# Kernel tuning notes

Hardware: AMD Instinct MI355X
Metric: run time of the kernel (lower is better)

## Reference

```python
import jax, jax.numpy as jnp
import numpy as np

B, STEP, H, N_ENC = 256, 32, 512, 60
PD, LD, NB, NTYPE, NPLAYER = 32, 32, 6, 11, 35


def _parity_masks(S):
    # Static relation-11/12 edge masks from update_adjacency_matrix (step is a Python int).
    m11 = np.zeros((S, S), dtype=bool)
    m12 = np.zeros((S, S), dtype=bool)
    for row in range(S):
        ni = row // 2
        if row % 2 == 0:
            c = (ni + 1) * 2
            if c <= S - 1:
                (m11 if ni % 2 == 0 else m12)[row, c] = True
                (m11 if ni % 2 == 0 else m12)[c, row] = True
        else:
            c = (ni + 1) * 2 + 1
            if c <= S - 1:
                (m12 if ni % 2 == 0 else m11)[row, c] = True
                (m12 if ni % 2 == 0 else m11)[c, row] = True
    return jnp.asarray(m11), jnp.asarray(m12)


def update_adjacency(adj, step, shot_type_predict=False):
    b = adj.shape[0]
    S = step * 2
    new = jnp.zeros((b, 13, S, S), dtype=adj.dtype).at[:, :, :S - 2, :S - 2].set(adj)
    m11, m12 = _parity_masks(S)
    new = new.at[:, 11].set(jnp.where(m11, 1, new[:, 11]))
    new = new.at[:, 12].set(jnp.where(m12, 1, new[:, 12]))
    if shot_type_predict:
        idx = (step - 1) * 2 if step % 2 == 0 else (step - 1) * 2 + 1
        new = new.at[:, :, idx, :].set(0).at[:, :, :, idx].set(0)
    return new


def rgcn(node, adj, layer_params):
    # adj: (B,13,N,N) int; slice off relation 0 -> 12 relations. Dropout is eval-mode identity.
    adj_f = adj[:, 1:].astype(node.dtype)  # (B,12,N,N)
    x = node
    n_layers = len(layer_params)
    for i, (basis, comb, w_self) in enumerate(layer_params):
        act = jax.nn.sigmoid if i == n_layers - 1 else jax.nn.relu
        W = jnp.einsum('rb,bij->rij', comb, basis)            # (12,H,H)
        msg = jnp.einsum('brnm,bmh->brnh', adj_f, x)          # (B,12,N,H)
        x = act(jnp.einsum('brnh,rhk->bnk', msg, W) + x @ w_self.T)
    return x


def setup_inputs() -> dict:
    key = jax.random.key(0)
    ks = jax.random.split(key, 20)
    s = 0.05
    return {
        'player': jax.random.randint(ks[0], (B, 2), 0, NPLAYER, dtype=jnp.int32),
        'step': STEP,
        'encode_node_embedding': jax.random.normal(ks[1], (B, N_ENC, H), jnp.float32),
        'adjacency_matrix': jax.random.randint(ks[2], (B, 13, (STEP - 1) * 2, (STEP - 1) * 2), 0, 2, dtype=jnp.int32),
        'player_A_x': jax.random.uniform(ks[3], (B, 1), jnp.float32),
        'player_A_y': jax.random.uniform(ks[4], (B, 1), jnp.float32),
        'player_B_x': jax.random.uniform(ks[5], (B, 1), jnp.float32),
        'player_B_y': jax.random.uniform(ks[6], (B, 1), jnp.float32),
        'emb_table': jax.random.normal(ks[7], (NPLAYER, PD), jnp.float32) * s,
        'coord_W': jax.random.normal(ks[8], (LD, 2), jnp.float32) * s,
        'coord_b': jnp.zeros((LD,), jnp.float32),
        'in_W': jax.random.normal(ks[9], (H, PD + LD), jnp.float32) * s,
        'in_b': jnp.zeros((H,), jnp.float32),
        'basis0': jax.random.normal(ks[10], (NB, H, H), jnp.float32) * s,
        'comb0': jax.random.normal(ks[11], (12, NB), jnp.float32) * s,
        'self0': jax.random.normal(ks[12], (H, H), jnp.float32) * s,
        'basis1': jax.random.normal(ks[13], (NB, H, H), jnp.float32) * s,
        'comb1': jax.random.normal(ks[14], (12, NB), jnp.float32) * s,
        'self1': jax.random.normal(ks[15], (H, H), jnp.float32) * s,
        'type_W': jax.random.normal(ks[16], (NTYPE, 2 * H), jnp.float32) * s,
        'type_b': jnp.zeros((NTYPE,), jnp.float32),
    }


def reference(player, step, encode_node_embedding, adjacency_matrix,
              player_A_x, player_A_y, player_B_x, player_B_y,
              emb_table, coord_W, coord_b, in_W, in_b,
              basis0, comb0, self0, basis1, comb1, self1, type_W, type_b):
    b = player.shape[0]
    layers = [(basis0, comb0, self0), (basis1, comb1, self1)]

    coord_A = jnp.stack([player_A_x, player_A_y], axis=2)   # (B,1,2)
    coord_B = jnp.stack([player_B_x, player_B_y], axis=2)   # (B,1,2)
    coords = jnp.stack([coord_A, coord_B], axis=2).reshape(b, -1, 2)  # (B,2,2)
    loc = jax.nn.relu(coords @ coord_W.T + coord_b)          # (B,2,LD)
    pemb = emb_table[player]                                 # (B,2,PD)
    initial = jnp.concatenate([loc, pemb], axis=-1) @ in_W.T + in_b  # (B,2,H)

    # first=False branch: current coords == prev coords, so model_input == initial
    mi = jnp.concatenate([encode_node_embedding, initial], axis=1)   # (B,62,H)
    tmp = rgcn(mi, adjacency_matrix, layers)
    passed = jnp.concatenate([encode_node_embedding[:, :-2], tmp[:, -4:]], axis=1)  # (B,62,H)

    tmp_adj = update_adjacency(adjacency_matrix, step, shot_type_predict=True)  # (B,13,64,64)
    mi2 = jnp.concatenate([passed, initial], axis=1)         # (B,64,H)
    drop = (step - 1) * 2 if step % 2 == 0 else (step - 1) * 2 + 1
    keep = np.delete(np.arange(step * 2), drop)
    mi2 = mi2[:, keep]
    tmp_adj = tmp_adj[:, :, keep][:, :, :, keep]
    tmp2 = rgcn(mi2, tmp_adj, layers)                        # (B,63,H)

    pad = jnp.zeros((b, tmp2.shape[1] + 1, tmp2.shape[2]), tmp2.dtype)
    if step % 2 == 0:
        pad = pad.at[:, :-2].set(tmp2[:, :-1]).at[:, -1].set(tmp2[:, -1])
    else:
        pad = pad.at[:, :-1].set(tmp2)
    stp = jnp.concatenate([passed[:, :-2], pad[:, -4:]], axis=1)  # (B,64,H)
    if step % 2 == 0:
        black = stp[:, (step - 1) * 2 + 1]
        white = stp[:, (step - 2) * 2]
    else:
        black = stp[:, (step - 2) * 2 + 1]
        white = stp[:, (step - 1) * 2]
    logits = jnp.concatenate([black, white], axis=-1) @ type_W.T + type_b
    return logits
```

## Files before the change

### kernel.cpp

```cpp
#include <hip/hip_runtime.h>
#include <hip/hip_bf16.h>

typedef unsigned short u16;
typedef unsigned long long u64;
typedef __attribute__((ext_vector_type(4))) short short4v;
typedef __attribute__((ext_vector_type(8))) short short8;
typedef __attribute__((ext_vector_type(4))) float floatx4;

__device__ __forceinline__ u16 f2bf(float f) {
    union { float f; unsigned u; } v; v.f = f;
    unsigned r = v.u + 0x7FFF + ((v.u >> 16) & 1);
    return (u16)(r >> 16);
}

__global__ void k_wcat(const float* __restrict__ basis, const float* __restrict__ selfW,
                       u16* __restrict__ wf) {
    int bi = blockIdx.x, t = threadIdx.x;
    int kr = t >> 7;
    int nb = (t & 127) * 4;
    for (int it = 0; it < 4; ++it) {
        int k = bi * 8 + it * 2 + kr;
        float v0, v1, v2, v3;
        if (k < 3072) {
            int q = k >> 9, h = k & 511;
            const float4 bz = *(const float4*)(basis + ((size_t)(q * 512 + h)) * 512 + nb);
            v0 = bz.x; v1 = bz.y; v2 = bz.z; v3 = bz.w;
        } else {
            int kk = k - 3072;
            v0 = selfW[(size_t)(nb + 0) * 512 + kk];
            v1 = selfW[(size_t)(nb + 1) * 512 + kk];
            v2 = selfW[(size_t)(nb + 2) * 512 + kk];
            v3 = selfW[(size_t)(nb + 3) * 512 + kk];
        }
        float vv[4] = {v0, v1, v2, v3};
        for (int i = 0; i < 4; ++i) {
            int n = nb + i;
            wf[(size_t)(k >> 5) * 16384 + (n >> 4) * 512 + ((k >> 3) & 3) * 128 + (n & 15) * 8 + (k & 7)] = f2bf(vv[i]);
        }
    }
}

__global__ void k_masks(const int* __restrict__ A, u64* __restrict__ m0, u64* __restrict__ m1) {
    int bi = blockIdx.x;
    int b = bi / 12, r = bi % 12;
    const int* Ab = A + (size_t)(b * 13 + (r + 1)) * 62 * 62;
    int lane = threadIdx.x;
    u64 my0 = 0, my1 = 0;
    for (int n = 0; n < 64; ++n) {
        int raw = 0;
        if (n < 62 && lane < 62) raw = (Ab[n * 62 + lane] != 0) ? 1 : 0;
        u64 b0 = __ballot(raw != 0);
        int v1 = 0;
        if (n < 63 && lane < 63) {
            int oi = (n == 62) ? 63 : n;
            int oj = (lane == 62) ? 63 : lane;
            v1 = (oi < 62 && oj < 62) ? raw : 0;
            int lo = (oi < oj) ? oi : oj, hi = (oi < oj) ? oj : oi;
            if (hi == lo + 2) {
                int p = (lo >> 1) & 1;
                int chp = ((lo & 1) == 0) ? (p ? 12 : 11) : (p ? 11 : 12);
                if (r + 1 == chp) v1 = 1;
            }
        }
        u64 b1 = __ballot(v1 != 0);
        if (lane == n) { my0 = b0; my1 = b1; }
    }
    m0[(size_t)bi * 64 + lane] = my0;
    m1[(size_t)bi * 64 + lane] = my1;
}

#define AQ_SETSTRIDE (256UL * 6 * 4096)
__global__ void k_aqexp(const u64* __restrict__ msk, const float* __restrict__ comb0,
                        const float* __restrict__ comb1, u16* __restrict__ aq) {
    int b = blockIdx.x >> 3, sp = blockIdx.x & 7;
    int t = threadIdx.x;
    __shared__ u64 sm[12 * 64];
    __shared__ float cmb[2][12][6];
    if (t < 72) { cmb[0][t / 6][t % 6] = comb0[t]; cmb[1][t / 6][t % 6] = comb1[t]; }
    for (int i = t; i < 768; i += 256) sm[i] = msk[(size_t)b * 768 + i];
    __syncthreads();
    #pragma unroll
    for (int ii2 = 0; ii2 < 2; ++ii2) {
        int pos = (sp * 2 + ii2) * 256 + t;
        int f = pos >> 9, lane = (pos >> 3) & 63, j = pos & 7;
        int row = ((f >> 1) << 4) + (lane & 15);
        int mb  = ((f & 1) << 5) + ((lane >> 4) << 3) + j;
        float bits[12];
        #pragma unroll
        for (int r = 0; r < 12; ++r) bits[r] = (float)((sm[r * 64 + row] >> mb) & 1ull);
        #pragma unroll
        for (int s = 0; s < 2; ++s)
            #pragma unroll
            for (int q = 0; q < 6; ++q) {
                float v = 0.f;
                #pragma unroll
                for (int r = 0; r < 12; ++r) v += bits[r] * cmb[s][r][q];
                aq[(size_t)s * AQ_SETSTRIDE + ((size_t)b * 6 + q) * 4096 + pos] = f2bf(v);
            }
    }
}

__global__ void k_prep(const int* __restrict__ player,
                       const float* __restrict__ pAx, const float* __restrict__ pAy,
                       const float* __restrict__ pBx, const float* __restrict__ pBy,
                       const float* __restrict__ emb, const float* __restrict__ cW,
                       const float* __restrict__ cb, const float* __restrict__ inW,
                       const float* __restrict__ inb,
                       u16* __restrict__ mi1, u16* __restrict__ mi2) {
    int b = blockIdx.x, t = threadIdx.x;
    __shared__ float feat[2][64];
    if (t < 64) {
        int j = t >> 5, d = t & 31;
        float X = j ? pBx[b] : pAx[b];
        float Y = j ? pBy[b] : pAy[b];
        feat[j][d] = fmaxf(cW[d * 2] * X + cW[d * 2 + 1] * Y + cb[d], 0.f);
        feat[j][32 + d] = emb[player[b * 2 + j] * 32 + d];
    }
    __syncthreads();
    for (int h = t; h < 512; h += 256) {
        float a0 = inb[h], a1 = inb[h];
        const float* wrow = inW + h * 64;
        #pragma unroll
        for (int d = 0; d < 64; ++d) {
            float wv = wrow[d];
            a0 += wv * feat[0][d];
            a1 += wv * feat[1][d];
        }
        u16 v0 = f2bf(a0), v1 = f2bf(a1);
        size_t base = (size_t)b * 64 * 512;
        mi1[base + 60 * 512 + h] = v0;
        mi1[base + 61 * 512 + h] = v1;
        mi1[base + 62 * 512 + h] = 0;
        mi1[base + 63 * 512 + h] = 0;
        mi2[base + 62 * 512 + h] = v1;
        mi2[base + 63 * 512 + h] = 0;
    }
}

__global__ void k_cast(const float* __restrict__ enc, u16* __restrict__ mi1, u16* __restrict__ mi2) {
    long long e = ((long long)blockIdx.x * 256 + threadIdx.x) * 8;
    if (e >= 256LL * 60 * 512) return;
    int b = (int)(e / (60 * 512));
    int rm = (int)(e % (60 * 512));
    int n = rm / 512, h = rm % 512;
    for (int i = 0; i < 8; ++i) {
        u16 v = f2bf(enc[e + i]);
        mi1[((size_t)b * 64 + n) * 512 + h + i] = v;
        if (n < 58) mi2[((size_t)b * 64 + n) * 512 + h + i] = v;
    }
}

__global__ __launch_bounds__(512, 2)
void k_layer(const u16* __restrict__ x, const u16* __restrict__ aq,
             const u16* __restrict__ wc, u16* __restrict__ out) {
    int b = blockIdx.x >> 1, nh = blockIdx.x & 1;
    int t = threadIdx.x, lane = t & 63, w = t >> 6;
    int l15 = lane & 15, lq = lane >> 4;
    const int TS = 520;
    __shared__ __align__(16) u16 T[64 * 520];

    const u16* xb_base = x + (size_t)b * 64 * 512;
    short8 xb[8];
    #pragma unroll
    for (int nt = 0; nt < 4; ++nt)
        #pragma unroll
        for (int kh = 0; kh < 2; ++kh) {
            int h = (w * 4 + nt) * 16 + l15;
            int j0 = kh * 32 + lq * 8;
            short8 v;
            #pragma unroll
            for (int jj = 0; jj < 8; ++jj)
                v[jj] = (short)xb_base[(size_t)(j0 + jj) * 512 + h];
            xb[nt * 2 + kh] = v;
        }

    floatx4 acc[8];
    #pragma unroll
    for (int i = 0; i < 8; ++i) acc[i] = (floatx4)(0.f);

    const u16* aqb   = aq + (size_t)b * 6 * 4096 + (size_t)lane * 8;
    const u16* wbase = wc + (size_t)lane * 8;
    int cf0 = nh * 16 + w * 2;

    for (int q = 0; q < 6; ++q) {
        __syncthreads();
        for (int i = 0; i < 4; ++i) {
            short8 a0 = *(const short8*)(aqb + (size_t)q * 4096 + (i * 2 + 0) * 512);
            short8 a1 = *(const short8*)(aqb + (size_t)q * 4096 + (i * 2 + 1) * 512);
            #pragma unroll
            for (int nt = 0; nt < 4; ++nt) {
                floatx4 tz = (floatx4)(0.f);
                tz = __builtin_amdgcn_mfma_f32_16x16x32_bf16(a0, xb[nt * 2 + 0], tz, 0, 0, 0);
                tz = __builtin_amdgcn_mfma_f32_16x16x32_bf16(a1, xb[nt * 2 + 1], tz, 0, 0, 0);
                int hcol = (w * 4 + nt) * 16 + l15;
                int mrow = i * 16 + lq * 4;
                #pragma unroll
                for (int reg = 0; reg < 4; ++reg)
                    T[(mrow + reg) * TS + hcol] = f2bf(tz[reg]);
            }
        }
        __syncthreads();
        for (int ks = 0; ks < 16; ++ks) {
            short8 af[4], bf[2];
            #pragma unroll
            for (int i = 0; i < 4; ++i)
                af[i] = *(const short8*)&T[(i * 16 + l15) * TS + ks * 32 + lq * 8];
            #pragma unroll
            for (int nt = 0; nt < 2; ++nt)
                bf[nt] = *(const short8*)(wbase + (size_t)(q * 16 + ks) * 16384 + (size_t)(cf0 + nt) * 512);
            #pragma unroll
            for (int i = 0; i < 4; ++i)
                #pragma unroll
                for (int nt = 0; nt < 2; ++nt)
                    acc[i * 2 + nt] = __builtin_amdgcn_mfma_f32_16x16x32_bf16(af[i], bf[nt], acc[i * 2 + nt], 0, 0, 0);
        }
    }
    for (int ks = 0; ks < 16; ++ks) {
        short8 af[4], bf[2];
        #pragma unroll
        for (int i = 0; i < 4; ++i)
            af[i] = *(const short8*)(xb_base + (size_t)(i * 16 + l15) * 512 + ks * 32 + lq * 8);
        #pragma unroll
        for (int nt = 0; nt < 2; ++nt)
            bf[nt] = *(const short8*)(wbase + (size_t)(96 + ks) * 16384 + (size_t)(cf0 + nt) * 512);
        #pragma unroll
        for (int i = 0; i < 4; ++i)
            #pragma unroll
            for (int nt = 0; nt < 2; ++nt)
                acc[i * 2 + nt] = __builtin_amdgcn_mfma_f32_16x16x32_bf16(af[i], bf[nt], acc[i * 2 + nt], 0, 0, 0);
    }
    #pragma unroll
    for (int i = 0; i < 4; ++i)
        #pragma unroll
        for (int nt = 0; nt < 2; ++nt) {
            int n = nh * 256 + w * 32 + nt * 16 + l15;
            int m0 = i * 16 + lq * 4;
            #pragma unroll
            for (int reg = 0; reg < 4; ++reg)
                out[((size_t)b * 64 + m0 + reg) * 512 + n] = f2bf(fmaxf(acc[i * 2 + nt][reg], 0.f));
        }
}

__global__ __launch_bounds__(512, 2)
void k_layer_last(const u16* __restrict__ x, const u16* __restrict__ aq,
                  const u16* __restrict__ wc, int mode,
                  u16* __restrict__ o16, float* __restrict__ o32) {
    int b = blockIdx.x >> 1, nh = blockIdx.x & 1;
    int t = threadIdx.x, lane = t & 63, w = t >> 6;
    int l15 = lane & 15, lq = lane >> 4;
    const int TS = 520;
    __shared__ __align__(16) u16 T[16 * 520];

    const u16* xb_base = x + (size_t)b * 64 * 512;
    short8 xb[8];
    #pragma unroll
    for (int nt = 0; nt < 4; ++nt)
        #pragma unroll
        for (int kh = 0; kh < 2; ++kh) {
            int h = (w * 4 + nt) * 16 + l15;
            int j0 = kh * 32 + lq * 8;
            short8 v;
            #pragma unroll
            for (int jj = 0; jj < 8; ++jj)
                v[jj] = (short)xb_base[(size_t)(j0 + jj) * 512 + h];
            xb[nt * 2 + kh] = v;
        }

    floatx4 acc[2];
    #pragma unroll
    for (int i = 0; i < 2; ++i) acc[i] = (floatx4)(0.f);

    const u16* aqb   = aq + (size_t)b * 6 * 4096 + (size_t)lane * 8;
    const u16* wbase = wc + (size_t)lane * 8;
    int cf0 = nh * 16 + w * 2;

    for (int q = 0; q < 6; ++q) {
        __syncthreads();
        {
            short8 a0 = *(const short8*)(aqb + (size_t)q * 4096 + 6 * 512);
            short8 a1 = *(const short8*)(aqb + (size_t)q * 4096 + 7 * 512);
            #pragma unroll
            for (int nt = 0; nt < 4; ++nt) {
                floatx4 tz = (floatx4)(0.f);
                tz = __builtin_amdgcn_mfma_f32_16x16x32_bf16(a0, xb[nt * 2 + 0], tz, 0, 0, 0);
                tz = __builtin_amdgcn_mfma_f32_16x16x32_bf16(a1, xb[nt * 2 + 1], tz, 0, 0, 0);
                int hcol = (w * 4 + nt) * 16 + l15;
                int mrow = lq * 4;
                #pragma unroll
                for (int reg = 0; reg < 4; ++reg)
                    T[(mrow + reg) * TS + hcol] = f2bf(tz[reg]);
            }
        }
        __syncthreads();
        for (int ks = 0; ks < 16; ++ks) {
            short8 af = *(const short8*)&T[l15 * TS + ks * 32 + lq * 8];
            #pragma unroll
            for (int nt = 0; nt < 2; ++nt) {
                short8 bf = *(const short8*)(wbase + (size_t)(q * 16 + ks) * 16384 + (size_t)(cf0 + nt) * 512);
                acc[nt] = __builtin_amdgcn_mfma_f32_16x16x32_bf16(af, bf, acc[nt], 0, 0, 0);
            }
        }
    }
    for (int ks = 0; ks < 16; ++ks) {
        short8 af = *(const short8*)(xb_base + (size_t)(48 + l15) * 512 + ks * 32 + lq * 8);
        #pragma unroll
        for (int nt = 0; nt < 2; ++nt) {
            short8 bf = *(const short8*)(wbase + (size_t)(96 + ks) * 16384 + (size_t)(cf0 + nt) * 512);
            acc[nt] = __builtin_amdgcn_mfma_f32_16x16x32_bf16(af, bf, acc[nt], 0, 0, 0);
        }
    }
    #pragma unroll
    for (int nt = 0; nt < 2; ++nt) {
        int n = nh * 256 + w * 32 + nt * 16 + l15;
        #pragma unroll
        for (int reg = 0; reg < 4; ++reg) {
            int m = 48 + lq * 4 + reg;
            float v = acc[nt][reg];
            if (mode == 1) {
                if (m >= 58 && m <= 61)
                    o16[((size_t)b * 64 + m) * 512 + n] = f2bf(1.f / (1.f + __expf(-v)));
            } else {
                if (m == 60 || m == 62) {
                    int slot = (m == 60) ? (b * 2) : (b * 2 + 1);
                    o32[(size_t)slot * 512 + n] = 1.f / (1.f + __expf(-v));
                }
            }
        }
    }
}

__global__ void k_final(const float* __restrict__ t2, const float* __restrict__ tW,
                        const float* __restrict__ tb, float* __restrict__ outp) {
    int b = blockIdx.x, l = threadIdx.x;
    float a[11];
    #pragma unroll
    for (int j = 0; j < 11; ++j) a[j] = 0.f;
    for (int it = 0; it < 16; ++it) {
        int h = it * 64 + l;
        float c = (h < 512) ? t2[(b * 2 + 1) * 512 + h] : t2[(b * 2 + 0) * 512 + (h - 512)];
        #pragma unroll
        for (int j = 0; j < 11; ++j) a[j] += c * tW[j * 1024 + h];
    }
    #pragma unroll
    for (int j = 0; j < 11; ++j) {
        float v = a[j];
        for (int off = 32; off > 0; off >>= 1) v += __shfl_down(v, off, 64);
        if (l == 0) outp[b * 11 + j] = v + tb[j];
    }
}

extern "C" void kernel_launch(void* const* d_in, const int* in_sizes, int n_in,
                              void* d_out, int out_size, void* d_ws, size_t ws_size,
                              hipStream_t stream) {
    const int*   player = (const int*)d_in[0];
    const float* enc    = (const float*)d_in[2];
    const int*   adjm   = (const int*)d_in[3];
    const float* pAx    = (const float*)d_in[4];
    const float* pAy    = (const float*)d_in[5];
    const float* pBx    = (const float*)d_in[6];
    const float* pBy    = (const float*)d_in[7];
    const float* emb    = (const float*)d_in[8];
    const float* cW     = (const float*)d_in[9];
    const float* cb     = (const float*)d_in[10];
    const float* inW    = (const float*)d_in[11];
    const float* inb    = (const float*)d_in[12];
    const float* basis0 = (const float*)d_in[13];
    const float* comb0  = (const float*)d_in[14];
    const float* self0  = (const float*)d_in[15];
    const float* basis1 = (const float*)d_in[16];
    const float* comb1  = (const float*)d_in[17];
    const float* self1  = (const float*)d_in[18];
    const float* typeW  = (const float*)d_in[19];
    const float* typeb  = (const float*)d_in[20];

    char* ws = (char*)d_ws;
    size_t off = 0;
    auto alloc = [&](size_t bytes) -> void* {
        void* p = ws + off;
        off = (off + bytes + 255) & ~(size_t)255;
        return p;
    };
    u16* mi1   = (u16*)alloc(256UL * 64 * 512 * 2);
    u16* mi2   = (u16*)alloc(256UL * 64 * 512 * 2);
    u16* x12   = (u16*)alloc(256UL * 64 * 512 * 2);
    u16* aqbuf = (u16*)alloc(2UL * AQ_SETSTRIDE * 2);
    u16* wcat0 = (u16*)alloc(3584UL * 512 * 2);
    u16* wcat1 = (u16*)alloc(3584UL * 512 * 2);
    u64* mm0   = (u64*)alloc(256UL * 12 * 64 * 8);
    u64* mm1   = (u64*)alloc(256UL * 12 * 64 * 8);
    u16* x12b  = mi1;
    float* t2  = (float*)x12;
    u16* aq0   = aqbuf;
    u16* aq1   = aqbuf + AQ_SETSTRIDE;

    k_wcat<<<448, 256, 0, stream>>>(basis0, self0, wcat0);
    k_wcat<<<448, 256, 0, stream>>>(basis1, self1, wcat1);
    k_masks<<<3072, 64, 0, stream>>>(adjm, mm0, mm1);
    k_aqexp<<<2048, 256, 0, stream>>>(mm0, comb0, comb1, aqbuf);
    k_prep<<<256, 256, 0, stream>>>(player, pAx, pAy, pBx, pBy, emb, cW, cb, inW, inb, mi1, mi2);
    k_cast<<<3840, 256, 0, stream>>>(enc, mi1, mi2);

    k_layer<<<512, 512, 0, stream>>>(mi1, aq0, wcat0, x12);
    k_layer_last<<<512, 512, 0, stream>>>(x12, aq1, wcat1, 1, mi2, nullptr);
    k_aqexp<<<2048, 256, 0, stream>>>(mm1, comb0, comb1, aqbuf);
    k_layer<<<512, 512, 0, stream>>>(mi2, aq0, wcat0, x12b);
    k_layer_last<<<512, 512, 0, stream>>>(x12b, aq1, wcat1, 2, nullptr, t2);

    k_final<<<256, 64, 0, stream>>>(t2, typeW, typeb, (float*)d_out);
}
```

Measured before the change: 605.7 us.

## Split RGCN layer kernels across more, smaller blocks and vectorize input cast

The layer kernel now runs 4 blocks per batch with 256 threads each, covering 128 output columns. It processes the hidden dimension in two halves so the shared staging tile shrinks to 64x264, and the self-weight GEMM moves to the start. The last-layer kernel splits across 8 blocks per batch and each wave holds a single accumulator. The cast kernel uses vectorized float4 loads and short8 stores. The aim is better occupancy and less shared memory per block, at the cost of recomputing the adjacency-times-x products in every column block and adding more syncs.

```diff
diff --git a/kernel.cpp b/kernel.cpp
--- a/kernel.cpp
+++ b/kernel.cpp
@@ -143,78 +143,35 @@
     int b = (int)(e / (60 * 512));
     int rm = (int)(e % (60 * 512));
     int n = rm / 512, h = rm % 512;
-    for (int i = 0; i < 8; ++i) {
-        u16 v = f2bf(enc[e + i]);
-        mi1[((size_t)b * 64 + n) * 512 + h + i] = v;
-        if (n < 58) mi2[((size_t)b * 64 + n) * 512 + h + i] = v;
-    }
-}
-
-__global__ __launch_bounds__(512, 2)
+    float4 f0 = *(const float4*)(enc + e);
+    float4 f1 = *(const float4*)(enc + e + 4);
+    short8 pk;
+    pk[0] = (short)f2bf(f0.x); pk[1] = (short)f2bf(f0.y);
+    pk[2] = (short)f2bf(f0.z); pk[3] = (short)f2bf(f0.w);
+    pk[4] = (short)f2bf(f1.x); pk[5] = (short)f2bf(f1.y);
+    pk[6] = (short)f2bf(f1.z); pk[7] = (short)f2bf(f1.w);
+    *(short8*)(mi1 + ((size_t)b * 64 + n) * 512 + h) = pk;
+    if (n < 58) *(short8*)(mi2 + ((size_t)b * 64 + n) * 512 + h) = pk;
+}
+
+__global__ __launch_bounds__(256, 4)
 void k_layer(const u16* __restrict__ x, const u16* __restrict__ aq,
              const u16* __restrict__ wc, u16* __restrict__ out) {
-    int b = blockIdx.x >> 1, nh = blockIdx.x & 1;
+    int b = blockIdx.x >> 2, cq = blockIdx.x & 3;
     int t = threadIdx.x, lane = t & 63, w = t >> 6;
     int l15 = lane & 15, lq = lane >> 4;
-    const int TS = 520;
-    __shared__ __align__(16) u16 T[64 * 520];
+    const int TS = 264;
+    __shared__ __align__(16) u16 T[64 * 264];
 
     const u16* xb_base = x + (size_t)b * 64 * 512;
-    short8 xb[8];
-    #pragma unroll
-    for (int nt = 0; nt < 4; ++nt)
-        #pragma unroll
-        for (int kh = 0; kh < 2; ++kh) {
-            int h = (w * 4 + nt) * 16 + l15;
-            int j0 = kh * 32 + lq * 8;
-            short8 v;
-            #pragma unroll
-            for (int jj = 0; jj < 8; ++jj)
-                v[jj] = (short)xb_base[(size_t)(j0 + jj) * 512 + h];
-            xb[nt * 2 + kh] = v;
-        }
-
-    floatx4 acc[8];
-    #pragma unroll
-    for (int i = 0; i < 8; ++i) acc[i] = (floatx4)(0.f);
-
     const u16* aqb   = aq + (size_t)b * 6 * 4096 + (size_t)lane * 8;
     const u16* wbase = wc + (size_t)lane * 8;
-    int cf0 = nh * 16 + w * 2;
-
-    for (int q = 0; q < 6; ++q) {
-        __syncthreads();
-        for (int i = 0; i < 4; ++i) {
-            short8 a0 = *(const short8*)(aqb + (size_t)q * 4096 + (i * 2 + 0) * 512);
-            short8 a1 = *(const short8*)(aqb + (size_t)q * 4096 + (i * 2 + 1) * 512);
-            #pragma unroll
-            for (int nt = 0; nt < 4; ++nt) {
-                floatx4 tz = (floatx4)(0.f);
-                tz = __builtin_amdgcn_mfma_f32_16x16x32_bf16(a0, xb[nt * 2 + 0], tz, 0, 0, 0);
-                tz = __builtin_amdgcn_mfma_f32_16x16x32_bf16(a1, xb[nt * 2 + 1], tz, 0, 0, 0);
-                int hcol = (w * 4 + nt) * 16 + l15;
-                int mrow = i * 16 + lq * 4;
-                #pragma unroll
-                for (int reg = 0; reg < 4; ++reg)
-                    T[(mrow + reg) * TS + hcol] = f2bf(tz[reg]);
-            }
-        }
-        __syncthreads();
-        for (int ks = 0; ks < 16; ++ks) {
-            short8 af[4], bf[2];
-            #pragma unroll
-            for (int i = 0; i < 4; ++i)
-                af[i] = *(const short8*)&T[(i * 16 + l15) * TS + ks * 32 + lq * 8];
-            #pragma unroll
-            for (int nt = 0; nt < 2; ++nt)
-                bf[nt] = *(const short8*)(wbase + (size_t)(q * 16 + ks) * 16384 + (size_t)(cf0 + nt) * 512);
-            #pragma unroll
-            for (int i = 0; i < 4; ++i)
-                #pragma unroll
-                for (int nt = 0; nt < 2; ++nt)
-                    acc[i * 2 + nt] = __builtin_amdgcn_mfma_f32_16x16x32_bf16(af[i], bf[nt], acc[i * 2 + nt], 0, 0, 0);
-        }
-    }
+    int cf0 = cq * 8 + w * 2;
+
+    floatx4 acc[8];
+    #pragma unroll
+    for (int i = 0; i < 8; ++i) acc[i] = (floatx4)(0.f);
+
     for (int ks = 0; ks < 16; ++ks) {
         short8 af[4], bf[2];
         #pragma unroll
@@ -229,11 +186,63 @@
             for (int nt = 0; nt < 2; ++nt)
                 acc[i * 2 + nt] = __builtin_amdgcn_mfma_f32_16x16x32_bf16(af[i], bf[nt], acc[i * 2 + nt], 0, 0, 0);
     }
+
+    for (int hh = 0; hh < 2; ++hh) {
+        short8 xb[8];
+        #pragma unroll
+        for (int nt = 0; nt < 4; ++nt)
+            #pragma unroll
+            for (int kh = 0; kh < 2; ++kh) {
+                int h = hh * 256 + w * 64 + nt * 16 + l15;
+                int j0 = kh * 32 + lq * 8;
+                short8 v;
+                #pragma unroll
+                for (int jj = 0; jj < 8; ++jj)
+                    v[jj] = (short)xb_base[(size_t)(j0 + jj) * 512 + h];
+                xb[nt * 2 + kh] = v;
+            }
+
+        for (int q = 0; q < 6; ++q) {
+            #pragma unroll
+            for (int i = 0; i < 4; ++i) {
+                short8 a0 = *(const short8*)(aqb + (size_t)q * 4096 + (i * 2 + 0) * 512);
+                short8 a1 = *(const short8*)(aqb + (size_t)q * 4096 + (i * 2 + 1) * 512);
+                #pragma unroll
+                for (int nt = 0; nt < 4; ++nt) {
+                    floatx4 tz = (floatx4)(0.f);
+                    tz = __builtin_amdgcn_mfma_f32_16x16x32_bf16(a0, xb[nt * 2 + 0], tz, 0, 0, 0);
+                    tz = __builtin_amdgcn_mfma_f32_16x16x32_bf16(a1, xb[nt * 2 + 1], tz, 0, 0, 0);
+                    int hcol = w * 64 + nt * 16 + l15;
+                    int mrow = i * 16 + lq * 4;
+                    #pragma unroll
+                    for (int reg = 0; reg < 4; ++reg)
+                        T[(mrow + reg) * TS + hcol] = f2bf(tz[reg]);
+                }
+            }
+            __syncthreads();
+            for (int kk = 0; kk < 8; ++kk) {
+                short8 af[4], bf[2];
+                #pragma unroll
+                for (int i = 0; i < 4; ++i)
+                    af[i] = *(const short8*)&T[(i * 16 + l15) * TS + kk * 32 + lq * 8];
+                #pragma unroll
+                for (int nt = 0; nt < 2; ++nt)
+                    bf[nt] = *(const short8*)(wbase + (size_t)(q * 16 + hh * 8 + kk) * 16384 + (size_t)(cf0 + nt) * 512);
+                #pragma unroll
+                for (int i = 0; i < 4; ++i)
+                    #pragma unroll
+                    for (int nt = 0; nt < 2; ++nt)
+                        acc[i * 2 + nt] = __builtin_amdgcn_mfma_f32_16x16x32_bf16(af[i], bf[nt], acc[i * 2 + nt], 0, 0, 0);
+            }
+            __syncthreads();
+        }
+    }
+
     #pragma unroll
     for (int i = 0; i < 4; ++i)
         #pragma unroll
         for (int nt = 0; nt < 2; ++nt) {
-            int n = nh * 256 + w * 32 + nt * 16 + l15;
+            int n = cq * 128 + w * 32 + nt * 16 + l15;
             int m0 = i * 16 + lq * 4;
             #pragma unroll
             for (int reg = 0; reg < 4; ++reg)
@@ -241,23 +250,35 @@
         }
 }
 
-__global__ __launch_bounds__(512, 2)
+__global__ __launch_bounds__(256, 4)
 void k_layer_last(const u16* __restrict__ x, const u16* __restrict__ aq,
                   const u16* __restrict__ wc, int mode,
                   u16* __restrict__ o16, float* __restrict__ o32) {
-    int b = blockIdx.x >> 1, nh = blockIdx.x & 1;
+    int b = blockIdx.x >> 3, ce = blockIdx.x & 7;
     int t = threadIdx.x, lane = t & 63, w = t >> 6;
     int l15 = lane & 15, lq = lane >> 4;
     const int TS = 520;
     __shared__ __align__(16) u16 T[16 * 520];
 
     const u16* xb_base = x + (size_t)b * 64 * 512;
-    short8 xb[8];
-    #pragma unroll
-    for (int nt = 0; nt < 4; ++nt)
+    const u16* aqb   = aq + (size_t)b * 6 * 4096 + (size_t)lane * 8;
+    const u16* wbase = wc + (size_t)lane * 8;
+    int cf = ce * 4 + w;
+
+    floatx4 acc = (floatx4)(0.f);
+
+    for (int ks = 0; ks < 16; ++ks) {
+        short8 af = *(const short8*)(xb_base + (size_t)(48 + l15) * 512 + ks * 32 + lq * 8);
+        short8 bf = *(const short8*)(wbase + (size_t)(96 + ks) * 16384 + (size_t)cf * 512);
+        acc = __builtin_amdgcn_mfma_f32_16x16x32_bf16(af, bf, acc, 0, 0, 0);
+    }
+
+    short8 xb[16];
+    #pragma unroll
+    for (int nt = 0; nt < 8; ++nt)
         #pragma unroll
         for (int kh = 0; kh < 2; ++kh) {
-            int h = (w * 4 + nt) * 16 + l15;
+            int h = w * 128 + nt * 16 + l15;
             int j0 = kh * 32 + lq * 8;
             short8 v;
             #pragma unroll
@@ -266,64 +287,41 @@
             xb[nt * 2 + kh] = v;
         }
 
-    floatx4 acc[2];
-    #pragma unroll
-    for (int i = 0; i < 2; ++i) acc[i] = (floatx4)(0.f);
-
-    const u16* aqb   = aq + (size_t)b * 6 * 4096 + (size_t)lane * 8;
-    const u16* wbase = wc + (size_t)lane * 8;
-    int cf0 = nh * 16 + w * 2;
-
     for (int q = 0; q < 6; ++q) {
-        __syncthreads();
-        {
-            short8 a0 = *(const short8*)(aqb + (size_t)q * 4096 + 6 * 512);
-            short8 a1 = *(const short8*)(aqb + (size_t)q * 4096 + 7 * 512);
-            #pragma unroll
-            for (int nt = 0; nt < 4; ++nt) {
-                floatx4 tz = (floatx4)(0.f);
-                tz = __builtin_amdgcn_mfma_f32_16x16x32_bf16(a0, xb[nt * 2 + 0], tz, 0, 0, 0);
-                tz = __builtin_amdgcn_mfma_f32_16x16x32_bf16(a1, xb[nt * 2 + 1], tz, 0, 0, 0);
-                int hcol = (w * 4 + nt) * 16 + l15;
-                int mrow = lq * 4;
-                #pragma unroll
-                for (int reg = 0; reg < 4; ++reg)
-                    T[(mrow + reg) * TS + hcol] = f2bf(tz[reg]);
-            }
+        short8 a0 = *(const short8*)(aqb + (size_t)q * 4096 + 6 * 512);
+        short8 a1 = *(const short8*)(aqb + (size_t)q * 4096 + 7 * 512);
+        #pragma unroll
+        for (int nt = 0; nt < 8; ++nt) {
+            floatx4 tz = (floatx4)(0.f);
+            tz = __builtin_amdgcn_mfma_f32_16x16x32_bf16(a0, xb[nt * 2 + 0], tz, 0, 0, 0);
+            tz = __builtin_amdgcn_mfma_f32_16x16x32_bf16(a1, xb[nt * 2 + 1], tz, 0, 0, 0);
+            int hcol = w * 128 + nt * 16 + l15;
+            int mrow = lq * 4;
+            #pragma unroll
+            for (int reg = 0; reg < 4; ++reg)
+                T[(mrow + reg) * TS + hcol] = f2bf(tz[reg]);
         }
         __syncthreads();
         for (int ks = 0; ks < 16; ++ks) {
             short8 af = *(const short8*)&T[l15 * TS + ks * 32 + lq * 8];
-            #pragma unroll
-            for (int nt = 0; nt < 2; ++nt) {
-                short8 bf = *(const short8*)(wbase + (size_t)(q * 16 + ks) * 16384 + (size_t)(cf0 + nt) * 512);
-                acc[nt] = __builtin_amdgcn_mfma_f32_16x16x32_bf16(af, bf, acc[nt], 0, 0, 0);
-            }
-        }
-    }
-    for (int ks = 0; ks < 16; ++ks) {
-        short8 af = *(const short8*)(xb_base + (size_t)(48 + l15) * 512 + ks * 32 + lq * 8);
-        #pragma unroll
-        for (int nt = 0; nt < 2; ++nt) {
-            short8 bf = *(const short8*)(wbase + (size_t)(96 + ks) * 16384 + (size_t)(cf0 + nt) * 512);
-            acc[nt] = __builtin_amdgcn_mfma_f32_16x16x32_bf16(af, bf, acc[nt], 0, 0, 0);
-        }
-    }
-    #pragma unroll
-    for (int nt = 0; nt < 2; ++nt) {
-        int n = nh * 256 + w * 32 + nt * 16 + l15;
-        #pragma unroll
-        for (int reg = 0; reg < 4; ++reg) {
-            int m = 48 + lq * 4 + reg;
-            float v = acc[nt][reg];
-            if (mode == 1) {
-                if (m >= 58 && m <= 61)
-                    o16[((size_t)b * 64 + m) * 512 + n] = f2bf(1.f / (1.f + __expf(-v)));
-            } else {
-                if (m == 60 || m == 62) {
-                    int slot = (m == 60) ? (b * 2) : (b * 2 + 1);
-                    o32[(size_t)slot * 512 + n] = 1.f / (1.f + __expf(-v));
-                }
+            short8 bf = *(const short8*)(wbase + (size_t)(q * 16 + ks) * 16384 + (size_t)cf * 512);
+            acc = __builtin_amdgcn_mfma_f32_16x16x32_bf16(af, bf, acc, 0, 0, 0);
+        }
+        __syncthreads();
+    }
+
+    int n = ce * 64 + w * 16 + l15;
+    #pragma unroll
+    for (int reg = 0; reg < 4; ++reg) {
+        int m = 48 + lq * 4 + reg;
+        float v = acc[reg];
+        if (mode == 1) {
+            if (m >= 58 && m <= 61)
+                o16[((size_t)b * 64 + m) * 512 + n] = f2bf(1.f / (1.f + __expf(-v)));
+        } else {
+            if (m == 60 || m == 62) {
+                int slot = (m == 60) ? (b * 2) : (b * 2 + 1);
+                o32[(size_t)slot * 512 + n] = 1.f / (1.f + __expf(-v));
             }
         }
     }
@@ -400,11 +398,11 @@
     k_prep<<<256, 256, 0, stream>>>(player, pAx, pAy, pBx, pBy, emb, cW, cb, inW, inb, mi1, mi2);
     k_cast<<<3840, 256, 0, stream>>>(enc, mi1, mi2);
 
-    k_layer<<<512, 512, 0, stream>>>(mi1, aq0, wcat0, x12);
-    k_layer_last<<<512, 512, 0, stream>>>(x12, aq1, wcat1, 1, mi2, nullptr);
+    k_layer<<<1024, 256, 0, stream>>>(mi1, aq0, wcat0, x12);
+    k_layer_last<<<2048, 256, 0, stream>>>(x12, aq1, wcat1, 1, mi2, nullptr);
     k_aqexp<<<2048, 256, 0, stream>>>(mm1, comb0, comb1, aqbuf);
-    k_layer<<<512, 512, 0, stream>>>(mi2, aq0, wcat0, x12b);
-    k_layer_last<<<512, 512, 0, stream>>>(x12b, aq1, wcat1, 2, nullptr, t2);
+    k_layer<<<1024, 256, 0, stream>>>(mi2, aq0, wcat0, x12b);
+    k_layer_last<<<2048, 256, 0, stream>>>(x12b, aq1, wcat1, 2, nullptr, t2);
 
     k_final<<<256, 64, 0, stream>>>(t2, typeW, typeb, (float*)d_out);
 }
```

Result: slower. 694.0 us (+14.6%).

## Restructure last RGCN layer with pre-transposed activations and smaller per-block tiles

Applied to the files above, without the earlier changes.

The first layer now writes its output in an MFMA-fragment-ready transposed layout plus a small row-major copy of the last 16 rows. The final-layer kernel is rewritten as single-wave blocks that load these fragments directly instead of doing strided element-wise transposes, with 8 column blocks per batch for more parallelism. The aq expansion keeps only the rows the last layer needs for the second set, and the setup kernels are merged (wcat pair, cast plus prep) with vectorized casting. The cost is two barriers per inner iteration in the new last-layer kernel, plus extra layout complexity.

```diff
diff --git a/kernel.cpp b/kernel.cpp
--- a/kernel.cpp
+++ b/kernel.cpp
@@ -13,9 +13,14 @@
     return (u16)(r >> 16);
 }
 
-__global__ void k_wcat(const float* __restrict__ basis, const float* __restrict__ selfW,
-                       u16* __restrict__ wf) {
+__global__ void k_wcat2(const float* __restrict__ b0, const float* __restrict__ s0,
+                        const float* __restrict__ b1, const float* __restrict__ s1,
+                        u16* __restrict__ wf0, u16* __restrict__ wf1) {
     int bi = blockIdx.x, t = threadIdx.x;
+    const float* basis = (bi < 448) ? b0 : b1;
+    const float* selfW = (bi < 448) ? s0 : s1;
+    u16* wf = (bi < 448) ? wf0 : wf1;
+    if (bi >= 448) bi -= 448;
     int kr = t >> 7;
     int nb = (t & 127) * 4;
     for (int it = 0; it < 4; ++it) {
@@ -69,9 +74,9 @@
     m1[(size_t)bi * 64 + lane] = my1;
 }
 
-#define AQ_SETSTRIDE (256UL * 6 * 4096)
 __global__ void k_aqexp(const u64* __restrict__ msk, const float* __restrict__ comb0,
-                        const float* __restrict__ comb1, u16* __restrict__ aq) {
+                        const float* __restrict__ comb1, u16* __restrict__ aq0,
+                        u16* __restrict__ aq1) {
     int b = blockIdx.x >> 3, sp = blockIdx.x & 7;
     int t = threadIdx.x;
     __shared__ u64 sm[12 * 64];
@@ -89,25 +94,45 @@
         #pragma unroll
         for (int r = 0; r < 12; ++r) bits[r] = (float)((sm[r * 64 + row] >> mb) & 1ull);
         #pragma unroll
-        for (int s = 0; s < 2; ++s)
-            #pragma unroll
-            for (int q = 0; q < 6; ++q) {
-                float v = 0.f;
-                #pragma unroll
-                for (int r = 0; r < 12; ++r) v += bits[r] * cmb[s][r][q];
-                aq[(size_t)s * AQ_SETSTRIDE + ((size_t)b * 6 + q) * 4096 + pos] = f2bf(v);
-            }
-    }
-}
-
-__global__ void k_prep(const int* __restrict__ player,
-                       const float* __restrict__ pAx, const float* __restrict__ pAy,
-                       const float* __restrict__ pBx, const float* __restrict__ pBy,
-                       const float* __restrict__ emb, const float* __restrict__ cW,
-                       const float* __restrict__ cb, const float* __restrict__ inW,
-                       const float* __restrict__ inb,
-                       u16* __restrict__ mi1, u16* __restrict__ mi2) {
-    int b = blockIdx.x, t = threadIdx.x;
+        for (int q = 0; q < 6; ++q) {
+            float v0 = 0.f, v1 = 0.f;
+            #pragma unroll
+            for (int r = 0; r < 12; ++r) {
+                v0 += bits[r] * cmb[0][r][q];
+                v1 += bits[r] * cmb[1][r][q];
+            }
+            aq0[((size_t)b * 6 + q) * 4096 + pos] = f2bf(v0);
+            if (f >= 6) aq1[((size_t)b * 6 + q) * 1024 + pos - 3072] = f2bf(v1);
+        }
+    }
+}
+
+__global__ void k_castprep(const float* __restrict__ enc,
+                           const int* __restrict__ player,
+                           const float* __restrict__ pAx, const float* __restrict__ pAy,
+                           const float* __restrict__ pBx, const float* __restrict__ pBy,
+                           const float* __restrict__ emb, const float* __restrict__ cW,
+                           const float* __restrict__ cb, const float* __restrict__ inW,
+                           const float* __restrict__ inb,
+                           u16* __restrict__ mi1, u16* __restrict__ mi2) {
+    int t = threadIdx.x;
+    if (blockIdx.x < 3840) {
+        long long e = ((long long)blockIdx.x * 256 + t) * 8;
+        int b = (int)(e / (60 * 512));
+        int rm = (int)(e % (60 * 512));
+        int n = rm / 512, h = rm % 512;
+        float4 f0 = *(const float4*)(enc + e);
+        float4 f1 = *(const float4*)(enc + e + 4);
+        short8 pk;
+        pk[0] = (short)f2bf(f0.x); pk[1] = (short)f2bf(f0.y);
+        pk[2] = (short)f2bf(f0.z); pk[3] = (short)f2bf(f0.w);
+        pk[4] = (short)f2bf(f1.x); pk[5] = (short)f2bf(f1.y);
+        pk[6] = (short)f2bf(f1.z); pk[7] = (short)f2bf(f1.w);
+        *(short8*)(mi1 + ((size_t)b * 64 + n) * 512 + h) = pk;
+        if (n < 58) *(short8*)(mi2 + ((size_t)b * 64 + n) * 512 + h) = pk;
+        return;
+    }
+    int b = blockIdx.x - 3840;
     __shared__ float feat[2][64];
     if (t < 64) {
         int j = t >> 5, d = t & 31;
@@ -137,22 +162,9 @@
     }
 }
 
-__global__ void k_cast(const float* __restrict__ enc, u16* __restrict__ mi1, u16* __restrict__ mi2) {
-    long long e = ((long long)blockIdx.x * 256 + threadIdx.x) * 8;
-    if (e >= 256LL * 60 * 512) return;
-    int b = (int)(e / (60 * 512));
-    int rm = (int)(e % (60 * 512));
-    int n = rm / 512, h = rm % 512;
-    for (int i = 0; i < 8; ++i) {
-        u16 v = f2bf(enc[e + i]);
-        mi1[((size_t)b * 64 + n) * 512 + h + i] = v;
-        if (n < 58) mi2[((size_t)b * 64 + n) * 512 + h + i] = v;
-    }
-}
-
 __global__ __launch_bounds__(512, 2)
 void k_layer(const u16* __restrict__ x, const u16* __restrict__ aq,
-             const u16* __restrict__ wc, u16* __restrict__ out) {
+             const u16* __restrict__ wc, u16* __restrict__ outT, u16* __restrict__ outR) {
     int b = blockIdx.x >> 1, nh = blockIdx.x & 1;
     int t = threadIdx.x, lane = t & 63, w = t >> 6;
     int l15 = lane & 15, lq = lane >> 4;
@@ -233,85 +245,85 @@
     for (int i = 0; i < 4; ++i)
         #pragma unroll
         for (int nt = 0; nt < 2; ++nt) {
-            int n = nh * 256 + w * 32 + nt * 16 + l15;
-            int m0 = i * 16 + lq * 4;
-            #pragma unroll
-            for (int reg = 0; reg < 4; ++reg)
-                out[((size_t)b * 64 + m0 + reg) * 512 + n] = f2bf(fmaxf(acc[i * 2 + nt][reg], 0.f));
-        }
-}
-
-__global__ __launch_bounds__(512, 2)
-void k_layer_last(const u16* __restrict__ x, const u16* __restrict__ aq,
-                  const u16* __restrict__ wc, int mode,
-                  u16* __restrict__ o16, float* __restrict__ o32) {
-    int b = blockIdx.x >> 1, nh = blockIdx.x & 1;
-    int t = threadIdx.x, lane = t & 63, w = t >> 6;
-    int l15 = lane & 15, lq = lane >> 4;
-    const int TS = 520;
-    __shared__ __align__(16) u16 T[16 * 520];
-
-    const u16* xb_base = x + (size_t)b * 64 * 512;
-    short8 xb[8];
-    #pragma unroll
-    for (int nt = 0; nt < 4; ++nt)
-        #pragma unroll
-        for (int kh = 0; kh < 2; ++kh) {
-            int h = (w * 4 + nt) * 16 + l15;
-            int j0 = kh * 32 + lq * 8;
-            short8 v;
-            #pragma unroll
-            for (int jj = 0; jj < 8; ++jj)
-                v[jj] = (short)xb_base[(size_t)(j0 + jj) * 512 + h];
-            xb[nt * 2 + kh] = v;
-        }
-
-    floatx4 acc[2];
-    #pragma unroll
-    for (int i = 0; i < 2; ++i) acc[i] = (floatx4)(0.f);
-
-    const u16* aqb   = aq + (size_t)b * 6 * 4096 + (size_t)lane * 8;
-    const u16* wbase = wc + (size_t)lane * 8;
-    int cf0 = nh * 16 + w * 2;
-
-    for (int q = 0; q < 6; ++q) {
-        __syncthreads();
-        {
-            short8 a0 = *(const short8*)(aqb + (size_t)q * 4096 + 6 * 512);
-            short8 a1 = *(const short8*)(aqb + (size_t)q * 4096 + 7 * 512);
-            #pragma unroll
-            for (int nt = 0; nt < 4; ++nt) {
-                floatx4 tz = (floatx4)(0.f);
-                tz = __builtin_amdgcn_mfma_f32_16x16x32_bf16(a0, xb[nt * 2 + 0], tz, 0, 0, 0);
-                tz = __builtin_amdgcn_mfma_f32_16x16x32_bf16(a1, xb[nt * 2 + 1], tz, 0, 0, 0);
-                int hcol = (w * 4 + nt) * 16 + l15;
-                int mrow = lq * 4;
+            short4v pk;
+            #pragma unroll
+            for (int reg = 0; reg < 4; ++reg) pk[reg] = (short)f2bf(fmaxf(acc[i * 2 + nt][reg], 0.f));
+            size_t a = (size_t)b * 32768 + (size_t)(i >> 1) * 16384 + (size_t)(cf0 + nt) * 512
+                     + (size_t)((i & 1) * 2 + (lq >> 1)) * 128 + (size_t)l15 * 8 + (lq & 1) * 4;
+            *(short4v*)(outT + a) = pk;
+            if (i == 3) {
+                int n = nh * 256 + w * 32 + nt * 16 + l15;
                 #pragma unroll
                 for (int reg = 0; reg < 4; ++reg)
-                    T[(mrow + reg) * TS + hcol] = f2bf(tz[reg]);
-            }
-        }
-        __syncthreads();
-        for (int ks = 0; ks < 16; ++ks) {
-            short8 af = *(const short8*)&T[l15 * TS + ks * 32 + lq * 8];
-            #pragma unroll
-            for (int nt = 0; nt < 2; ++nt) {
-                short8 bf = *(const short8*)(wbase + (size_t)(q * 16 + ks) * 16384 + (size_t)(cf0 + nt) * 512);
+                    outR[((size_t)b * 16 + lq * 4 + reg) * 512 + n] = (u16)pk[reg];
+            }
+        }
+}
+
+__global__ __launch_bounds__(64)
+void k_klast(const u16* __restrict__ xT, const u16* __restrict__ xr,
+             const u16* __restrict__ aq1, const u16* __restrict__ wc, int mode,
+             u16* __restrict__ o16, float* __restrict__ o32) {
+    int b = blockIdx.x >> 3, cb = blockIdx.x & 7;
+    int lane = threadIdx.x;
+    int l15 = lane & 15, lq = lane >> 4;
+    const int PS = 40;
+    __shared__ __align__(16) u16 tp[16 * 40];
+
+    const u16* xTb   = xT + (size_t)b * 32768 + (size_t)lane * 8;
+    const u16* wbase = wc + (size_t)lane * 8;
+    const u16* aqb   = aq1 + (size_t)b * 6 * 1024 + (size_t)lane * 8;
+
+    short8 aqf[12];
+    #pragma unroll
+    for (int q = 0; q < 6; ++q) {
+        aqf[q * 2 + 0] = *(const short8*)(aqb + (size_t)q * 1024);
+        aqf[q * 2 + 1] = *(const short8*)(aqb + (size_t)q * 1024 + 512);
+    }
+
+    floatx4 acc[4];
+    #pragma unroll
+    for (int i = 0; i < 4; ++i) acc[i] = (floatx4)(0.f);
+
+    for (int ks = 0; ks < 16; ++ks) {
+        short8 af = *(const short8*)(xr + ((size_t)b * 16 + l15) * 512 + ks * 32 + lq * 8);
+        #pragma unroll
+        for (int nt = 0; nt < 4; ++nt) {
+            short8 bf = *(const short8*)(wbase + (size_t)(96 + ks) * 16384 + (size_t)(cb * 4 + nt) * 512);
+            acc[nt] = __builtin_amdgcn_mfma_f32_16x16x32_bf16(af, bf, acc[nt], 0, 0, 0);
+        }
+    }
+
+    for (int p = 0; p < 16; ++p) {
+        short8 xb00 = *(const short8*)(xTb + (size_t)(2 * p + 0) * 512);
+        short8 xb01 = *(const short8*)(xTb + 16384 + (size_t)(2 * p + 0) * 512);
+        short8 xb10 = *(const short8*)(xTb + (size_t)(2 * p + 1) * 512);
+        short8 xb11 = *(const short8*)(xTb + 16384 + (size_t)(2 * p + 1) * 512);
+        for (int q = 0; q < 6; ++q) {
+            floatx4 tz0 = (floatx4)(0.f), tz1 = (floatx4)(0.f);
+            tz0 = __builtin_amdgcn_mfma_f32_16x16x32_bf16(aqf[q * 2 + 0], xb00, tz0, 0, 0, 0);
+            tz0 = __builtin_amdgcn_mfma_f32_16x16x32_bf16(aqf[q * 2 + 1], xb01, tz0, 0, 0, 0);
+            tz1 = __builtin_amdgcn_mfma_f32_16x16x32_bf16(aqf[q * 2 + 0], xb10, tz1, 0, 0, 0);
+            tz1 = __builtin_amdgcn_mfma_f32_16x16x32_bf16(aqf[q * 2 + 1], xb11, tz1, 0, 0, 0);
+            #pragma unroll
+            for (int reg = 0; reg < 4; ++reg) {
+                tp[(lq * 4 + reg) * PS + l15]      = f2bf(tz0[reg]);
+                tp[(lq * 4 + reg) * PS + 16 + l15] = f2bf(tz1[reg]);
+            }
+            __syncthreads();
+            short8 af = *(const short8*)&tp[l15 * PS + lq * 8];
+            __syncthreads();
+            #pragma unroll
+            for (int nt = 0; nt < 4; ++nt) {
+                short8 bf = *(const short8*)(wbase + (size_t)(q * 16 + p) * 16384 + (size_t)(cb * 4 + nt) * 512);
                 acc[nt] = __builtin_amdgcn_mfma_f32_16x16x32_bf16(af, bf, acc[nt], 0, 0, 0);
             }
         }
     }
-    for (int ks = 0; ks < 16; ++ks) {
-        short8 af = *(const short8*)(xb_base + (size_t)(48 + l15) * 512 + ks * 32 + lq * 8);
-        #pragma unroll
-        for (int nt = 0; nt < 2; ++nt) {
-            short8 bf = *(const short8*)(wbase + (size_t)(96 + ks) * 16384 + (size_t)(cf0 + nt) * 512);
-            acc[nt] = __builtin_amdgcn_mfma_f32_16x16x32_bf16(af, bf, acc[nt], 0, 0, 0);
-        }
-    }
-    #pragma unroll
-    for (int nt = 0; nt < 2; ++nt) {
-        int n = nh * 256 + w * 32 + nt * 16 + l15;
+
+    #pragma unroll
+    for (int nt = 0; nt < 4; ++nt) {
+        int n = cb * 64 + nt * 16 + l15;
         #pragma unroll
         for (int reg = 0; reg < 4; ++reg) {
             int m = 48 + lq * 4 + reg;
@@ -382,29 +394,26 @@
     };
     u16* mi1   = (u16*)alloc(256UL * 64 * 512 * 2);
     u16* mi2   = (u16*)alloc(256UL * 64 * 512 * 2);
-    u16* x12   = (u16*)alloc(256UL * 64 * 512 * 2);
-    u16* aqbuf = (u16*)alloc(2UL * AQ_SETSTRIDE * 2);
+    u16* x12T  = (u16*)alloc(256UL * 32768 * 2);
+    u16* x12r  = (u16*)alloc(256UL * 16 * 512 * 2);
+    u16* aq0   = (u16*)alloc(256UL * 6 * 4096 * 2);
+    u16* aq1   = (u16*)alloc(256UL * 6 * 1024 * 2);
     u16* wcat0 = (u16*)alloc(3584UL * 512 * 2);
     u16* wcat1 = (u16*)alloc(3584UL * 512 * 2);
     u64* mm0   = (u64*)alloc(256UL * 12 * 64 * 8);
     u64* mm1   = (u64*)alloc(256UL * 12 * 64 * 8);
-    u16* x12b  = mi1;
-    float* t2  = (float*)x12;
-    u16* aq0   = aqbuf;
-    u16* aq1   = aqbuf + AQ_SETSTRIDE;
-
-    k_wcat<<<448, 256, 0, stream>>>(basis0, self0, wcat0);
-    k_wcat<<<448, 256, 0, stream>>>(basis1, self1, wcat1);
+    float* t2  = (float*)mi1;
+
+    k_wcat2<<<896, 256, 0, stream>>>(basis0, self0, basis1, self1, wcat0, wcat1);
     k_masks<<<3072, 64, 0, stream>>>(adjm, mm0, mm1);
-    k_aqexp<<<2048, 256, 0, stream>>>(mm0, comb0, comb1, aqbuf);
-    k_prep<<<256, 256, 0, stream>>>(player, pAx, pAy, pBx, pBy, emb, cW, cb, inW, inb, mi1, mi2);
-    k_cast<<<3840, 256, 0, stream>>>(enc, mi1, mi2);
-
-    k_layer<<<512, 512, 0, stream>>>(mi1, aq0, wcat0, x12);
-    k_layer_last<<<512, 512, 0, stream>>>(x12, aq1, wcat1, 1, mi2, nullptr);
-    k_aqexp<<<2048, 256, 0, stream>>>(mm1, comb0, comb1, aqbuf);
-    k_layer<<<512, 512, 0, stream>>>(mi2, aq0, wcat0, x12b);
-    k_layer_last<<<512, 512, 0, stream>>>(x12b, aq1, wcat1, 2, nullptr, t2);
+    k_aqexp<<<2048, 256, 0, stream>>>(mm0, comb0, comb1, aq0, aq1);
+    k_castprep<<<4096, 256, 0, stream>>>(enc, player, pAx, pAy, pBx, pBy, emb, cW, cb, inW, inb, mi1, mi2);
+
+    k_layer<<<512, 512, 0, stream>>>(mi1, aq0, wcat0, x12T, x12r);
+    k_klast<<<2048, 64, 0, stream>>>(x12T, x12r, aq1, wcat1, 1, mi2, nullptr);
+    k_aqexp<<<2048, 256, 0, stream>>>(mm1, comb0, comb1, aq0, aq1);
+    k_layer<<<512, 512, 0, stream>>>(mi2, aq0, wcat0, x12T, x12r);
+    k_klast<<<2048, 64, 0, stream>>>(x12T, x12r, aq1, wcat1, 2, nullptr, t2);
 
     k_final<<<256, 64, 0, stream>>>(t2, typeW, typeb, (float*)d_out);
 }
```

Result: slower. 723.3 us (+19.4%).
